# Kernel tuning notes

Measured on AMD Instinct MI355X. Metric: run time of the kernel, lower is better.

## Reference

```python
import jax, jax.numpy as jnp
import numpy as np

N, E, B = 20000, 320000, 64
NODE_DIM, HID, HEADS, L, EMB = 128, 256, 4, 3, 256
C = HID // HEADS
NEG_SLOPE = 0.2
LN_EPS = 1e-5


def setup_inputs() -> dict:
    key = jax.random.key(0)
    ks = jax.random.split(key, 12)
    inp = {
        'x': jax.random.normal(ks[0], (N, NODE_DIM), jnp.float32),
        'edge_index': jax.random.randint(ks[1], (2, E), 0, N, jnp.int32),
        'batch': ((jnp.arange(N, dtype=jnp.int32) * B) // N).astype(jnp.int32),
        'W_in': jax.random.normal(ks[2], (NODE_DIM, HID), jnp.float32) * 0.05,
        'b_in': jnp.zeros((HID,), jnp.float32),
        'cls_token': jax.random.normal(ks[3], (HID,), jnp.float32),
        'W_gat': jax.random.normal(ks[4], (L, HID, HID), jnp.float32) * 0.05,
        'att_src': jax.random.normal(ks[5], (L, HEADS, C), jnp.float32) * 0.1,
        'att_dst': jax.random.normal(ks[6], (L, HEADS, C), jnp.float32) * 0.1,
        'b_gat': jnp.zeros((L, HID), jnp.float32),
        'ln_g': jnp.ones((L, HID), jnp.float32),
        'ln_b': jnp.zeros((L, HID), jnp.float32),
        'W_out': jax.random.normal(ks[7], (HID, EMB), jnp.float32) * 0.05,
        'b_out': jnp.zeros((EMB,), jnp.float32),
    }
    return inp


def _layer_norm(h, g, b):
    mu = jnp.mean(h, axis=-1, keepdims=True)
    var = jnp.mean(jnp.square(h - mu), axis=-1, keepdims=True)
    return (h - mu) * jax.lax.rsqrt(var + LN_EPS) * g + b


def _gat_layer(h, src, dst, n_nodes, W, a_s, a_d, bias):
    # PyG GATConv: shared linear, per-head attention, softmax over incoming edges
    xs = (h @ W).reshape(n_nodes, HEADS, C)          # (N',H,C)
    al_s = jnp.sum(xs * a_s, axis=-1)                # (N',H)
    al_d = jnp.sum(xs * a_d, axis=-1)                # (N',H)
    e = jax.nn.leaky_relu(al_s[src] + al_d[dst], NEG_SLOPE)  # (E',H)
    m = jax.ops.segment_max(e, dst, num_segments=n_nodes)
    ex = jnp.exp(e - m[dst])
    den = jax.ops.segment_sum(ex, dst, num_segments=n_nodes)
    alpha = ex / (den[dst] + 1e-16)                  # (E',H)
    msg = alpha[:, :, None] * xs[src]                # (E',H,C)
    out = jax.ops.segment_sum(msg, dst, num_segments=n_nodes)
    return out.reshape(n_nodes, HID) + bias


def reference(x, edge_index, batch, W_in, b_in, cls_token, W_gat, att_src,
              att_dst, b_gat, ln_g, ln_b, W_out, b_out):
    n_new = B + N
    h = x @ W_in + b_in                              # (N,HID)
    cls = jnp.broadcast_to(cls_token[None, :], (B, HID))
    h = jnp.concatenate([cls, h], axis=0)            # (B+N,HID)
    # build augmented edge list: shifted edges + bidirectional CLS edges + self loops
    src0 = edge_index[0] + B
    dst0 = edge_index[1] + B
    node_idx = jnp.arange(N, dtype=jnp.int32) + B
    cls_idx = batch
    loops = jnp.arange(n_new, dtype=jnp.int32)
    src = jnp.concatenate([src0, cls_idx, node_idx, loops])
    dst = jnp.concatenate([dst0, node_idx, cls_idx, loops])
    for l in range(L):
        g = _gat_layer(h, src, dst, n_new, W_gat[l], att_src[l], att_dst[l], b_gat[l])
        h = _layer_norm(h + g, ln_g[l], ln_b[l])
    z_e = h[:B] @ W_out + b_out                      # (B,EMB)
    return z_e
```

## Files before the change

kernel.cpp:

```cpp
#include <hip/hip_runtime.h>
#include <hip/hip_bf16.h>

constexpr int HID = 256;
constexpr int CAP = 64;
constexpr float NEG = 0.2f;
constexpr float EPS = 1e-5f;

typedef __attribute__((ext_vector_type(8))) short bf16x8;
typedef __attribute__((ext_vector_type(4))) float f32x4;

static __device__ __forceinline__ unsigned short f2bf(float f) {
    unsigned u = __builtin_bit_cast(unsigned, f);
    u += 0x7fffu + ((u >> 16) & 1u);
    return (unsigned short)(u >> 16);
}
static __device__ __forceinline__ float bf2f(unsigned short h) {
    return __builtin_bit_cast(float, ((unsigned)h) << 16);
}
static __device__ __forceinline__ float elk(float v) {
    v = v > 0.f ? v : NEG * v;
    return __expf(v);
}


__device__ __forceinline__ void frag_task(const float* __restrict__ W,
                                          ushort* __restrict__ out,
                                          int KS, int nmat, int q) {
    int per = KS * 1024;
    if (q >= per * nmat) return;
    int mat = q / per, r = q - mat * per;
    int l = r & 63, nf = (r >> 6) & 15, kk = r >> 10;
    const float* Wm = W + (size_t)mat * KS * 32 * 256;
    int kb = kk * 32 + ((l >> 4) << 3);
    int col = nf * 16 + (l & 15);
    bf16x8 v;
#pragma unroll
    for (int j = 0; j < 8; ++j) v[j] = (short)f2bf(Wm[(size_t)(kb + j) * 256 + col]);
    *(bf16x8*)(out + (size_t)q * 8) = v;
}

__global__ void k_pre(const float* __restrict__ x, ushort* __restrict__ xb,
                      const float* __restrict__ cls, ushort* __restrict__ h0,
                      const float* __restrict__ W_in, ushort* __restrict__ wf_in,
                      const float* __restrict__ W_gat, ushort* __restrict__ wf_gat,
                      const int* __restrict__ batch, int* lo, int* hi,
                      int* cursor, int* csr, int N, int B, int n_new) {
    int bid = blockIdx.x, t = threadIdx.x;
    const int nb_cvt  = (N * 128 / 4 + 255) / 256;
    const int nb_init = (n_new + 255) / 256;
    const int nb_csr  = (n_new * CAP + 255) / 256;
    const int nb_bnd  = (N + 255) / 256;
    const int nb_cls  = (B * HID / 4 + 255) / 256;
    const int nb_fin  = (4 * 1024 + 255) / 256;

    if (bid < nb_cvt) {
        int i = bid * 256 + t;
        int n4 = N * 128 / 4;
        if (i < n4) {
            float4 v = ((const float4*)x)[i];
            ushort4 o;
            o.x = f2bf(v.x); o.y = f2bf(v.y); o.z = f2bf(v.z); o.w = f2bf(v.w);
            ((ushort4*)xb)[i] = o;
        }
        return;
    }
    bid -= nb_cvt;
    if (bid < nb_init) {
        int i = bid * 256 + t;
        if (i < n_new) cursor[i] = 0;
        return;
    }
    bid -= nb_init;
    if (bid < nb_csr) {
        int i = bid * 256 + t;
        if (i < n_new * CAP) csr[i] = -1;
        return;
    }
    bid -= nb_csr;
    if (bid < nb_bnd) {
        int i = bid * 256 + t;
        if (i < N) {
            int b = batch[i];
            if (i == 0 || batch[i - 1] != b) lo[b] = i;
            if (i == N - 1 || batch[i + 1] != b) hi[b] = i + 1;
        }
        return;
    }
    bid -= nb_bnd;
    if (bid < nb_cls) {
        int i = bid * 256 + t;
        if (i < B * HID / 4) {
            int ch = (i & 63) * 4;
            ushort4 o;
            o.x = f2bf(cls[ch]); o.y = f2bf(cls[ch + 1]);
            o.z = f2bf(cls[ch + 2]); o.w = f2bf(cls[ch + 3]);
            ((ushort4*)h0)[i] = o;
        }
        return;
    }
    bid -= nb_cls;
    if (bid < nb_fin) {
        frag_task(W_in, wf_in, 4, 1, bid * 256 + t);
        return;
    }
    bid -= nb_fin;
    frag_task(W_gat, wf_gat, 8, 3, bid * 256 + t);
}


__global__ void k_fill(const int* __restrict__ src0, const int* __restrict__ dst0,
                       int* cursor, int* __restrict__ csr, int E, int B) {
    int e = blockIdx.x * blockDim.x + threadIdx.x;
    if (e < E) {
        int d = dst0[e] + B;
        int p = atomicAdd(&cursor[d], 1);
        if (p < CAP) csr[d * CAP + p] = src0[e] + B;
    }
}


__global__ void k_alpha(const int* __restrict__ csr, const int* __restrict__ cursor,
                        const float* __restrict__ als, const float* __restrict__ ald,
                        const int* __restrict__ batch,
                        float* __restrict__ a4T, float* __restrict__ acls,
                        float* __restrict__ aself, float* __restrict__ aclsinT,
                        int n_new, int B) {
    const int NSLOT = n_new * CAP;
    int i = blockIdx.x * 256 + threadIdx.x;
    if (i < NSLOT) {
        int d = i >> 6, p = i & (CAP - 1);
        int deg = cursor[d];
        deg = deg < CAP ? deg : CAP;
        int degp = (deg + 7) & ~7;
        if (p >= degp) return;
        int s = csr[i];
        float ox = 0.f, oy = 0.f, oz = 0.f, ow = 0.f;
        if (s >= 0) {
            float4 s4 = ((const float4*)als)[s];
            float4 d4 = ((const float4*)ald)[d];
            ox = elk(s4.x + d4.x);
            oy = elk(s4.y + d4.y);
            oz = elk(s4.z + d4.z);
            ow = elk(s4.w + d4.w);
        }
        a4T[i] = ox;
        a4T[(size_t)NSLOT + i] = oy;
        a4T[(size_t)2 * NSLOT + i] = oz;
        a4T[(size_t)3 * NSLOT + i] = ow;
        return;
    }
    int n = i - NSLOT;
    if (n < n_new) {
        float4 d4 = ((const float4*)ald)[n];
        float4 s4 = ((const float4*)als)[n];
        float4 o;
        o.x = elk(s4.x + d4.x);
        o.y = elk(s4.y + d4.y);
        o.z = elk(s4.z + d4.z);
        o.w = elk(s4.w + d4.w);
        ((float4*)aself)[n] = o;
        if (n >= B) {
            int c = batch[n - B];
            float4 cs = ((const float4*)als)[c];
            float4 p4;
            p4.x = elk(cs.x + d4.x);
            p4.y = elk(cs.y + d4.y);
            p4.z = elk(cs.z + d4.z);
            p4.w = elk(cs.w + d4.w);
            ((float4*)acls)[n] = p4;
            float4 cd = ((const float4*)ald)[c];
            aclsinT[n] = elk(s4.x + cd.x);
            aclsinT[(size_t)n_new + n] = elk(s4.y + cd.y);
            aclsinT[(size_t)2 * n_new + n] = elk(s4.z + cd.z);
            aclsinT[(size_t)3 * n_new + n] = elk(s4.w + cd.w);
        }
    }
}


template <int KS, bool ATT, bool BIAS>
__global__ __launch_bounds__(256, 4) void k_mgemm(
    const ushort* __restrict__ A, const ushort* __restrict__ Wf,
    const float* __restrict__ bias, ushort* __restrict__ outb,
    const float* __restrict__ att_s, const float* __restrict__ att_d,
    float* __restrict__ al_s, float* __restrict__ al_d, int rows)
{
    constexpr int K = KS * 32;
    int lane = threadIdx.x & 63, w = threadIdx.x >> 6;
    int rbase = blockIdx.x * 32;
    int arow0 = rbase + (lane & 15);
    int kofs = (lane >> 4) << 3;

    f32x4 acc[2][4];
#pragma unroll
    for (int mf = 0; mf < 2; ++mf)
#pragma unroll
        for (int nf = 0; nf < 4; ++nf) acc[mf][nf] = (f32x4){0.f, 0.f, 0.f, 0.f};

    const ushort* a0p = A + (size_t)arow0 * K + kofs;
    const ushort* a1p = a0p + (size_t)16 * K;
    bool g0 = arow0 < rows, g1 = (arow0 + 16) < rows;

#pragma unroll
    for (int kk = 0; kk < KS; ++kk) {
        bf16x8 af0 = {0, 0, 0, 0, 0, 0, 0, 0}, af1 = {0, 0, 0, 0, 0, 0, 0, 0};
        if (g0) af0 = *(const bf16x8*)(a0p + kk * 32);
        if (g1) af1 = *(const bf16x8*)(a1p + kk * 32);
        const bf16x8* wp = ((const bf16x8*)Wf) + (size_t)(kk * 16 + 4 * w) * 64 + lane;
#pragma unroll
        for (int nf = 0; nf < 4; ++nf) {
            bf16x8 bv = wp[nf * 64];
            acc[0][nf] = __builtin_amdgcn_mfma_f32_16x16x32_bf16(af0, bv, acc[0][nf], 0, 0, 0);
            acc[1][nf] = __builtin_amdgcn_mfma_f32_16x16x32_bf16(af1, bv, acc[1][nf], 0, 0, 0);
        }
    }

    int rg = (lane >> 4) * 4;
    int c0 = lane & 15;
    int colbase = w * 64;
    float bv[4];
    if (BIAS) {
#pragma unroll
        for (int nf = 0; nf < 4; ++nf) bv[nf] = bias[colbase + nf * 16 + c0];
    }
#pragma unroll
    for (int mf = 0; mf < 2; ++mf)
#pragma unroll
        for (int r = 0; r < 4; ++r) {
            int row = rbase + mf * 16 + rg + r;
            if (row < rows) {
#pragma unroll
                for (int nf = 0; nf < 4; ++nf) {
                    float v = acc[mf][nf][r];
                    if (BIAS) v += bv[nf];
                    outb[(size_t)row * HID + colbase + nf * 16 + c0] = f2bf(v);
                }
            }
        }

    if (ATT) {
        float as[4], ad[4];
#pragma unroll
        for (int nf = 0; nf < 4; ++nf) {
            as[nf] = att_s[colbase + nf * 16 + c0];
            ad[nf] = att_d[colbase + nf * 16 + c0];
        }
#pragma unroll
        for (int mf = 0; mf < 2; ++mf)
#pragma unroll
            for (int r = 0; r < 4; ++r) {
                float ps = 0.f, pd = 0.f;
#pragma unroll
                for (int nf = 0; nf < 4; ++nf) {
                    float v = acc[mf][nf][r];
                    ps += v * as[nf];
                    pd += v * ad[nf];
                }
#pragma unroll
                for (int o = 1; o < 16; o <<= 1) {
                    ps += __shfl_xor(ps, o, 64);
                    pd += __shfl_xor(pd, o, 64);
                }
                int row = rbase + mf * 16 + rg + r;
                if (c0 == 0 && row < rows) {
                    al_s[row * 4 + w] = ps;
                    al_d[row * 4 + w] = pd;
                }
            }
    }
}


__global__ __launch_bounds__(256, 4) void k_agg(
    const ushort* __restrict__ hb, const ushort* __restrict__ xs,
    const float* __restrict__ a4T, const float* __restrict__ acls,
    const float* __restrict__ aself, const float* __restrict__ aclsinT,
    const int* __restrict__ cursor, const int* __restrict__ csr,
    const int* __restrict__ batch, const int* __restrict__ lo,
    const int* __restrict__ hi,
    const float* __restrict__ b_gat, const float* __restrict__ ln_g,
    const float* __restrict__ ln_b,
    ushort* __restrict__ h_out, int n_new, int B)
{
    int t = threadIdx.x, w = t >> 6, lane = t & 63;
    int n = blockIdx.x * 4 + w;
    if (n >= n_new) return;
    int es = lane >> 5, cg = lane & 31, head = cg >> 3;
    const int NSLOT = n_new * CAP;

    float acc[8] = {0.f, 0.f, 0.f, 0.f, 0.f, 0.f, 0.f, 0.f};
    float den = 0.f;

    if (n >= B) {
        int gdeg = cursor[n];
        gdeg = gdeg < CAP ? gdeg : CAP;
        int gdegp = (gdeg + 7) & ~7;
        int clssrc = batch[n - B];
        bf16x8 xcls  = *((const bf16x8*)(xs + (size_t)clssrc * HID) + cg);
        bf16x8 xself = *((const bf16x8*)(xs + (size_t)n * HID) + cg);
        float acl = acls[n * 4 + head];
        float asf = aself[n * 4 + head];

        const int4* cp = (const int4*)(csr + n * CAP);
        const float4* ap = (const float4*)(a4T + (size_t)head * NSLOT + (size_t)n * CAP);
#pragma unroll 2
        for (int eb = 0; eb < gdegp; eb += 8) {
            int idx = (eb >> 2) + es;
            int4 s4 = cp[idx];
            float4 av = ap[idx];
            int s0 = s4.x < 0 ? 0 : s4.x;
            int s1 = s4.y < 0 ? 0 : s4.y;
            int s2 = s4.z < 0 ? 0 : s4.z;
            int s3 = s4.w < 0 ? 0 : s4.w;
            bf16x8 x0 = *((const bf16x8*)(xs + (size_t)s0 * HID) + cg);
            bf16x8 x1 = *((const bf16x8*)(xs + (size_t)s1 * HID) + cg);
            bf16x8 x2 = *((const bf16x8*)(xs + (size_t)s2 * HID) + cg);
            bf16x8 x3 = *((const bf16x8*)(xs + (size_t)s3 * HID) + cg);
            den += av.x + av.y + av.z + av.w;
#pragma unroll
            for (int j = 0; j < 8; ++j) {
                acc[j] += av.x * bf2f((unsigned short)x0[j]);
                acc[j] += av.y * bf2f((unsigned short)x1[j]);
                acc[j] += av.z * bf2f((unsigned short)x2[j]);
                acc[j] += av.w * bf2f((unsigned short)x3[j]);
            }
        }
        if (es == 0) {
            den += acl + asf;
#pragma unroll
            for (int j = 0; j < 8; ++j)
                acc[j] += acl * bf2f((unsigned short)xcls[j]) +
                          asf * bf2f((unsigned short)xself[j]);
        }
    } else {
        int cb = B + lo[n], cdeg = hi[n] - lo[n];
        bf16x8 xself = *((const bf16x8*)(xs + (size_t)n * HID) + cg);
        float asf = aself[n * 4 + head];
        const float* wp = aclsinT + (size_t)head * n_new;
        for (int eb = 0; eb < cdeg; eb += 8) {
            int b0 = eb + es * 4;
#pragma unroll
            for (int k = 0; k < 4; ++k) {
                int e = b0 + k;
                int ec = e < cdeg ? e : cdeg - 1;
                int src = cb + ec;
                float a = e < cdeg ? wp[src] : 0.f;
                bf16x8 xv = *((const bf16x8*)(xs + (size_t)src * HID) + cg);
                den += a;
#pragma unroll
                for (int j = 0; j < 8; ++j) acc[j] += a * bf2f((unsigned short)xv[j]);
            }
        }
        if (es == 0) {
            den += asf;
#pragma unroll
            for (int j = 0; j < 8; ++j) acc[j] += asf * bf2f((unsigned short)xself[j]);
        }
    }

#pragma unroll
    for (int j = 0; j < 8; ++j) acc[j] += __shfl_xor(acc[j], 32, 64);
    den += __shfl_xor(den, 32, 64);
    float inv = 1.f / (den + 1e-16f);

    bf16x8 hv = *((const bf16x8*)(hb + (size_t)n * HID) + cg);
    const float4* bgp = (const float4*)(b_gat + cg * 8);
    float4 bg0 = bgp[0], bg1 = bgp[1];
    float bg[8] = {bg0.x, bg0.y, bg0.z, bg0.w, bg1.x, bg1.y, bg1.z, bg1.w};
    float r[8];
#pragma unroll
    for (int j = 0; j < 8; ++j)
        r[j] = bf2f((unsigned short)hv[j]) + acc[j] * inv + bg[j];

    float ss = 0.f;
#pragma unroll
    for (int j = 0; j < 8; ++j) ss += r[j];
#pragma unroll
    for (int o = 1; o < 32; o <<= 1) ss += __shfl_xor(ss, o, 64);
    float mu = ss * (1.f / HID);
    float vv = 0.f;
#pragma unroll
    for (int j = 0; j < 8; ++j) { r[j] -= mu; vv += r[j] * r[j]; }
#pragma unroll
    for (int o = 1; o < 32; o <<= 1) vv += __shfl_xor(vv, o, 64);
    float rs = rsqrtf(vv * (1.f / HID) + EPS);

    if (es == 0) {
        const float4* gp = (const float4*)(ln_g + cg * 8);
        const float4* bp = (const float4*)(ln_b + cg * 8);
        float4 g0 = gp[0], g1 = gp[1];
        float4 lb0 = bp[0], lb1 = bp[1];
        float gg[8] = {g0.x, g0.y, g0.z, g0.w, g1.x, g1.y, g1.z, g1.w};
        float bb[8] = {lb0.x, lb0.y, lb0.z, lb0.w, lb1.x, lb1.y, lb1.z, lb1.w};
        bf16x8 o8;
#pragma unroll
        for (int j = 0; j < 8; ++j) o8[j] = (short)f2bf(r[j] * rs * gg[j] + bb[j]);
        *((bf16x8*)(h_out + (size_t)n * HID) + cg) = o8;
    }
}


__global__ __launch_bounds__(256) void k_out(
    const ushort* __restrict__ h, const float* __restrict__ Wm,
    const float* __restrict__ bias, float* __restrict__ z)
{
    __shared__ float hs[HID];
    int b = blockIdx.x, t = threadIdx.x;
    hs[t] = bf2f(h[(size_t)b * HID + t]);
    __syncthreads();
    float acc = bias[t];
#pragma unroll 8
    for (int k = 0; k < HID; ++k) acc += hs[k] * Wm[k * HID + t];
    z[(size_t)b * HID + t] = acc;
}


extern "C" void kernel_launch(void* const* d_in, const int* in_sizes, int n_in,
                              void* d_out, int out_size, void* d_ws, size_t ws_size,
                              hipStream_t stream) {
    const float* x      = (const float*)d_in[0];
    const int*   ei     = (const int*)d_in[1];
    const int*   batch  = (const int*)d_in[2];
    const float* W_in   = (const float*)d_in[3];
    const float* b_in   = (const float*)d_in[4];
    const float* cls    = (const float*)d_in[5];
    const float* W_gat  = (const float*)d_in[6];
    const float* att_s  = (const float*)d_in[7];
    const float* att_d  = (const float*)d_in[8];
    const float* b_gat  = (const float*)d_in[9];
    const float* ln_g   = (const float*)d_in[10];
    const float* ln_b   = (const float*)d_in[11];
    const float* W_out  = (const float*)d_in[12];
    const float* b_out  = (const float*)d_in[13];

    const int N = in_sizes[0] / 128;
    const int E = in_sizes[1] / 2;
    const int B = 64;
    const int n_new = N + B;
    const int* src0 = ei;
    const int* dst0 = ei + E;

    char* p = (char*)d_ws;
    auto alloc = [&](size_t bytes) -> void* {
        void* r = (void*)p;
        p += (bytes + 255) & ~(size_t)255;
        return r;
    };
    int*    cursor = (int*)alloc((size_t)n_new * 4);
    int*    csr    = (int*)alloc((size_t)n_new * CAP * 4);
    int*    lo     = (int*)alloc((size_t)B * 4);
    int*    hi     = (int*)alloc((size_t)B * 4);
    ushort* xb     = (ushort*)alloc((size_t)N * 128 * 2);
    ushort* h0b    = (ushort*)alloc((size_t)n_new * HID * 2);
    ushort* h1b    = (ushort*)alloc((size_t)n_new * HID * 2);
    ushort* xsb    = (ushort*)alloc((size_t)n_new * HID * 2);
    float*  als    = (float*)alloc((size_t)n_new * 4 * 4);
    float*  aldv   = (float*)alloc((size_t)n_new * 4 * 4);
    float*  a4T    = (float*)alloc((size_t)n_new * CAP * 4 * 4);
    float*  acls   = (float*)alloc((size_t)n_new * 4 * 4);
    float*  aselfv = (float*)alloc((size_t)n_new * 4 * 4);
    float*  aclsinT= (float*)alloc((size_t)n_new * 4 * 4);
    ushort* wf_in  = (ushort*)alloc((size_t)4 * 1024 * 8 * 2);
    ushort* wf_gat = (ushort*)alloc((size_t)3 * 8 * 1024 * 8 * 2);

    const int nb_pre = (N * 128 / 4 + 255) / 256 + (n_new + 255) / 256 +
                       (n_new * CAP + 255) / 256 + (N + 255) / 256 +
                       (B * HID / 4 + 255) / 256 +
                       (4 * 1024 + 255) / 256 + (3 * 8 * 1024 + 255) / 256;
    k_pre<<<nb_pre, 256, 0, stream>>>(x, xb, cls, h0b, W_in, wf_in, W_gat, wf_gat,
                                      batch, lo, hi, cursor, csr, N, B, n_new);
    k_fill<<<(E + 255) / 256, 256, 0, stream>>>(src0, dst0, cursor, csr, E, B);

    k_mgemm<4, false, true><<<(N + 31) / 32, 256, 0, stream>>>(
        xb, wf_in, b_in, h0b + (size_t)B * HID, nullptr, nullptr, nullptr, nullptr, N);

    const int nb_alpha = (n_new * CAP + n_new + 255) / 256;
    ushort* cur = h0b;
    ushort* nxt = h1b;
    for (int l = 0; l < 3; ++l) {
        k_mgemm<8, true, false><<<(n_new + 31) / 32, 256, 0, stream>>>(
            cur, wf_gat + (size_t)l * 65536, nullptr, xsb,
            att_s + l * HID, att_d + l * HID, als, aldv, n_new);
        k_alpha<<<nb_alpha, 256, 0, stream>>>(
            csr, cursor, als, aldv, batch, a4T, acls, aselfv, aclsinT, n_new, B);
        k_agg<<<(n_new + 3) / 4, 256, 0, stream>>>(
            cur, xsb, a4T, acls, aselfv, aclsinT, cursor, csr, batch, lo, hi,
            b_gat + l * HID, ln_g + l * HID, ln_b + l * HID, nxt, n_new, B);
        ushort* tmp = cur; cur = nxt; nxt = tmp;
    }
    k_out<<<B, 256, 0, stream>>>(cur, W_out, b_out, (float*)d_out);
}
```

Measured before the change: 213.9 us.

## Compute only CLS-node aggregation in the final GAT layer

The output reads only the B CLS rows after the last layer, so layer 3 now skips the per-edge alpha computation and full-graph aggregation. A new k_aggcls kernel aggregates each CLS node's incoming member-node messages plus its self loop and applies layer norm, launched over B blocks. k_alpha gains a template flag to compute only self and CLS terms. This removes most of one layer's edge work but depends on CLS nodes receiving edges only from their contiguous batch range and their self loop.

```diff
diff --git a/kernel.cpp b/kernel.cpp
--- a/kernel.cpp
+++ b/kernel.cpp
@@ -119,6 +119,7 @@
 }
 
 
+template <bool SLOTS>
 __global__ void k_alpha(const int* __restrict__ csr, const int* __restrict__ cursor,
                         const float* __restrict__ als, const float* __restrict__ ald,
                         const int* __restrict__ batch,
@@ -127,29 +128,32 @@
                         int n_new, int B) {
     const int NSLOT = n_new * CAP;
     int i = blockIdx.x * 256 + threadIdx.x;
-    if (i < NSLOT) {
-        int d = i >> 6, p = i & (CAP - 1);
-        int deg = cursor[d];
-        deg = deg < CAP ? deg : CAP;
-        int degp = (deg + 7) & ~7;
-        if (p >= degp) return;
-        int s = csr[i];
-        float ox = 0.f, oy = 0.f, oz = 0.f, ow = 0.f;
-        if (s >= 0) {
-            float4 s4 = ((const float4*)als)[s];
-            float4 d4 = ((const float4*)ald)[d];
-            ox = elk(s4.x + d4.x);
-            oy = elk(s4.y + d4.y);
-            oz = elk(s4.z + d4.z);
-            ow = elk(s4.w + d4.w);
-        }
-        a4T[i] = ox;
-        a4T[(size_t)NSLOT + i] = oy;
-        a4T[(size_t)2 * NSLOT + i] = oz;
-        a4T[(size_t)3 * NSLOT + i] = ow;
-        return;
-    }
-    int n = i - NSLOT;
+    if (SLOTS) {
+        if (i < NSLOT) {
+            int d = i >> 6, p = i & (CAP - 1);
+            int deg = cursor[d];
+            deg = deg < CAP ? deg : CAP;
+            int degp = (deg + 7) & ~7;
+            if (p >= degp) return;
+            int s = csr[i];
+            float ox = 0.f, oy = 0.f, oz = 0.f, ow = 0.f;
+            if (s >= 0) {
+                float4 s4 = ((const float4*)als)[s];
+                float4 d4 = ((const float4*)ald)[d];
+                ox = elk(s4.x + d4.x);
+                oy = elk(s4.y + d4.y);
+                oz = elk(s4.z + d4.z);
+                ow = elk(s4.w + d4.w);
+            }
+            a4T[i] = ox;
+            a4T[(size_t)NSLOT + i] = oy;
+            a4T[(size_t)2 * NSLOT + i] = oz;
+            a4T[(size_t)3 * NSLOT + i] = ow;
+            return;
+        }
+        i -= NSLOT;
+    }
+    int n = i;
     if (n < n_new) {
         float4 d4 = ((const float4*)ald)[n];
         float4 s4 = ((const float4*)als)[n];
@@ -400,6 +404,76 @@
 }
 
 
+__global__ __launch_bounds__(256) void k_aggcls(
+    const ushort* __restrict__ hb, const ushort* __restrict__ xs,
+    const float* __restrict__ aself, const float* __restrict__ aclsinT,
+    const int* __restrict__ lo, const int* __restrict__ hi,
+    const float* __restrict__ b_gat, const float* __restrict__ ln_g,
+    const float* __restrict__ ln_b,
+    ushort* __restrict__ h_out, int n_new, int B)
+{
+    __shared__ float sacc[4][256];
+    __shared__ float sden[4][4];
+    __shared__ float red[8];
+    int b = blockIdx.x;
+    int t = threadIdx.x, w = t >> 6, lane = t & 63;
+    int es = lane >> 5, cg = lane & 31, head = cg >> 3;
+
+    int cb = B + lo[b], cdeg = hi[b] - lo[b];
+    const float* wp = aclsinT + (size_t)head * n_new;
+
+    float acc[8] = {0.f, 0.f, 0.f, 0.f, 0.f, 0.f, 0.f, 0.f};
+    float den = 0.f;
+    for (int eb = w * 8; eb < cdeg; eb += 32) {
+        int b0 = eb + es * 4;
+#pragma unroll
+        for (int k = 0; k < 4; ++k) {
+            int e = b0 + k;
+            int ec = e < cdeg ? e : cdeg - 1;
+            int src = cb + ec;
+            float a = e < cdeg ? wp[src] : 0.f;
+            bf16x8 xv = *((const bf16x8*)(xs + (size_t)src * HID) + cg);
+            den += a;
+#pragma unroll
+            for (int j = 0; j < 8; ++j) acc[j] += a * bf2f((unsigned short)xv[j]);
+        }
+    }
+#pragma unroll
+    for (int j = 0; j < 8; ++j) acc[j] += __shfl_xor(acc[j], 32, 64);
+    den += __shfl_xor(den, 32, 64);
+    if (es == 0) {
+#pragma unroll
+        for (int j = 0; j < 8; ++j) sacc[w][cg * 8 + j] = acc[j];
+        if ((cg & 7) == 0) sden[w][head] = den;
+    }
+    __syncthreads();
+
+    int c = t, hh = c >> 6;
+    float atot = sacc[0][c] + sacc[1][c] + sacc[2][c] + sacc[3][c];
+    float dtot = sden[0][hh] + sden[1][hh] + sden[2][hh] + sden[3][hh];
+    float asf = aself[b * 4 + hh];
+    atot += asf * bf2f(xs[(size_t)b * HID + c]);
+    dtot += asf;
+    float r = bf2f(hb[(size_t)b * HID + c]) + atot / (dtot + 1e-16f) + b_gat[c];
+
+    float s1 = r;
+#pragma unroll
+    for (int o = 32; o > 0; o >>= 1) s1 += __shfl_xor(s1, o, 64);
+    if (lane == 0) red[w] = s1;
+    __syncthreads();
+    float mu = (red[0] + red[1] + red[2] + red[3]) * (1.f / HID);
+    float d = r - mu;
+    float v2 = d * d;
+#pragma unroll
+    for (int o = 32; o > 0; o >>= 1) v2 += __shfl_xor(v2, o, 64);
+    if (lane == 0) red[4 + w] = v2;
+    __syncthreads();
+    float var = (red[4] + red[5] + red[6] + red[7]) * (1.f / HID);
+    float rs = rsqrtf(var + EPS);
+    h_out[(size_t)b * HID + c] = f2bf(d * rs * ln_g[c] + ln_b[c]);
+}
+
+
 __global__ __launch_bounds__(256) void k_out(
     const ushort* __restrict__ h, const float* __restrict__ Wm,
     const float* __restrict__ bias, float* __restrict__ z)
@@ -481,11 +555,19 @@
         k_mgemm<8, true, false><<<(n_new + 31) / 32, 256, 0, stream>>>(
             cur, wf_gat + (size_t)l * 65536, nullptr, xsb,
             att_s + l * HID, att_d + l * HID, als, aldv, n_new);
-        k_alpha<<<nb_alpha, 256, 0, stream>>>(
-            csr, cursor, als, aldv, batch, a4T, acls, aselfv, aclsinT, n_new, B);
-        k_agg<<<(n_new + 3) / 4, 256, 0, stream>>>(
-            cur, xsb, a4T, acls, aselfv, aclsinT, cursor, csr, batch, lo, hi,
-            b_gat + l * HID, ln_g + l * HID, ln_b + l * HID, nxt, n_new, B);
+        if (l < 2) {
+            k_alpha<true><<<nb_alpha, 256, 0, stream>>>(
+                csr, cursor, als, aldv, batch, a4T, acls, aselfv, aclsinT, n_new, B);
+            k_agg<<<(n_new + 3) / 4, 256, 0, stream>>>(
+                cur, xsb, a4T, acls, aselfv, aclsinT, cursor, csr, batch, lo, hi,
+                b_gat + l * HID, ln_g + l * HID, ln_b + l * HID, nxt, n_new, B);
+        } else {
+            k_alpha<false><<<(n_new + 255) / 256, 256, 0, stream>>>(
+                csr, cursor, als, aldv, batch, a4T, acls, aselfv, aclsinT, n_new, B);
+            k_aggcls<<<B, 256, 0, stream>>>(
+                cur, xsb, aselfv, aclsinT, lo, hi,
+                b_gat + l * HID, ln_g + l * HID, ln_b + l * HID, nxt, n_new, B);
+        }
         ushort* tmp = cur; cur = nxt; nxt = tmp;
     }
     k_out<<<B, 256, 0, stream>>>(cur, W_out, b_out, (float*)d_out);
```

Measured after the change: 188.5 us (median of 2 runs). -11.9%, faster.
